# Kernel tuning notes

Measured on AMD Instinct MI355X. Metric: run time of the kernel, lower is better.

## Reference

```python
import jax, jax.numpy as jnp
import numpy as np
from jax import lax

T = 131072  # num frames
PARENTS = [-1, 0, 0, 1, 2, 3, 4, 5, 6]          # lower-body kinematic tree
LOWER_BODY = [0, 1, 2, 4, 5, 7, 8, 10, 11]      # SMPL joint ids of the 9 lower-body joints
FEET = [7, 5, 8, 6]                              # left toe, left heel, right toe, right heel (lower-body local ids)
FLOOR_Y = -0.93                                  # min y of ankle/foot joints in SMPL zero pose
GRAVITY_VELOCITY = -0.0018


def setup_inputs() -> dict:
    key = jax.random.key(0)
    k1, k2, k3 = jax.random.split(key, 3)
    pose = jax.random.normal(k1, (T, 24, 3, 3), dtype=jnp.float32)
    bone = 0.2 * jax.random.normal(k2, (9, 3), dtype=jnp.float32)
    bone = bone.at[:3].set(0.0)  # root + hip offsets zeroed, as in __init__ (b[:3] = 0)
    index = jax.random.randint(k3, (T,), 0, 4, dtype=jnp.int32)
    return {"pose": pose, "lower_body_bone": bone, "index": index}


def _forward_kinematics(pose_lower, bone):
    # pose_lower: [T, 9, 3, 3] local rotations; bone: [9, 3] bone offsets.
    # R_global[i] = R_global[parent] @ R_local[i];  p[i] = p[parent] + R_global[parent] @ bone[i]
    Rg = [pose_lower[:, 0]]
    p = [jnp.broadcast_to(bone[0], (pose_lower.shape[0], 3))]
    for i in range(1, 9):
        pa = PARENTS[i]
        Rg.append(jnp.einsum('tij,tjk->tik', Rg[pa], pose_lower[:, i]))
        p.append(p[pa] + jnp.einsum('tij,j->ti', Rg[pa], bone[i]))
    return jnp.stack(p, axis=1)  # [T, 9, 3]


def reference(pose, lower_body_bone, index):
    gravity = jnp.array([0.0, GRAVITY_VELOCITY, 0.0], dtype=pose.dtype)
    pose_lower = pose[:, jnp.array(LOWER_BODY)]               # [T, 9, 3, 3]
    j = _forward_kinematics(pose_lower, lower_body_bone)      # [T, 9, 3]

    # per-foot velocities: j[t-1] - j[t], zero at t=0  -> [T, 4, 3]
    feet = j[:, jnp.array(FEET)]                              # [T, 4, 3]
    vel_full = jnp.concatenate([jnp.zeros((1, 4, 3), dtype=j.dtype), feet[:-1] - feet[1:]], axis=0)
    vel_select = jnp.take_along_axis(vel_full, index[:, None, None].astype(jnp.int32), axis=1)[:, 0]  # [T, 3]
    velocity = gravity + vel_select                           # [T, 3]

    # sequential floor-contact correction on the y component
    foot_min_y = jnp.min(j[:, 5:9, 1], axis=1)                # [T]

    def step(root_y, inp):
        vy, fmin = inp
        foot_y = root_y + fmin
        vy_new = jnp.where(foot_y + vy <= FLOOR_Y, FLOOR_Y - foot_y, vy)
        return root_y + vy_new, vy_new

    _, vy_all = lax.scan(step, jnp.asarray(0.0, dtype=j.dtype), (velocity[:, 1], foot_min_y))
    velocity = velocity.at[:, 1].set(vy_all)

    trans = jnp.cumsum(velocity, axis=0)                      # velocity_to_root_position
    return pose, trans
```

## Files before the change

### kernel.cpp

```cpp
#include <hip/hip_runtime.h>
#include <math.h>

#define T_TOTAL   131072
#define POSE_FLTS (131072 * 216)
#define BT        64
#define NB        (T_TOTAL / BT)
#define F4PB      (BT * 54)
#define TS_LDS    84
#define FLOOR_YC  (-0.93f)
#define GRAV_Y    (-0.0018f)
#define NEG_INF   (-INFINITY)

typedef float floatx4 __attribute__((ext_vector_type(4)));


__device__ __forceinline__ void mat3mul(const float* A, const float* B, float* C) {
#pragma unroll
    for (int r = 0; r < 3; ++r) {
#pragma unroll
        for (int c = 0; c < 3; ++c) {
            C[r * 3 + c] = fmaf(A[r * 3 + 2], B[6 + c],
                           fmaf(A[r * 3 + 1], B[3 + c],
                                A[r * 3 + 0] * B[c]));
        }
    }
}

__device__ __forceinline__ void mva(const float* R, const float* b,
                                    const float* pin, float* pout) {
#pragma unroll
    for (int r = 0; r < 3; ++r) {
        pout[r] = pin[r] + fmaf(R[r * 3 + 2], b[2],
                            fmaf(R[r * 3 + 1], b[1], R[r * 3 + 0] * b[0]));
    }
}

__device__ __forceinline__ float sel_foot(const float f[12], int idx, int c) {
    float r = f[0 + c];
    r = (idx == 1) ? f[3 + c] : r;
    r = (idx == 2) ? f[6 + c] : r;
    r = (idx == 3) ? f[9 + c] : r;
    return r;
}

__device__ __forceinline__ void fk_feet(const float* __restrict__ P,
                                        const float* __restrict__ bone,
                                        float feet[12], float* fmin) {
    float Pl[84];
    const floatx4* p4 = (const floatx4*)P;
#pragma unroll
    for (int i = 0; i < 7; ++i) {
        floatx4 q = p4[i];
        Pl[4*i] = q.x; Pl[4*i+1] = q.y; Pl[4*i+2] = q.z; Pl[4*i+3] = q.w;
    }
#pragma unroll
    for (int i = 9; i < 14; ++i) {
        floatx4 q = p4[i];
        Pl[4*i] = q.x; Pl[4*i+1] = q.y; Pl[4*i+2] = q.z; Pl[4*i+3] = q.w;
    }
#pragma unroll
    for (int i = 15; i < 21; ++i) {
        floatx4 q = p4[i];
        Pl[4*i] = q.x; Pl[4*i+1] = q.y; Pl[4*i+2] = q.z; Pl[4*i+3] = q.w;
    }

    const float* M0 = Pl + 0;
    const float* M1 = Pl + 9;
    const float* M2 = Pl + 18;
    const float* M3 = Pl + 36;
    const float* M4 = Pl + 45;
    const float* M5 = Pl + 63;
    const float* M6 = Pl + 72;

    float R1[9], R2[9], R3[9], R4[9], R5[9], R6[9];
    mat3mul(M0, M1, R1);
    mat3mul(M0, M2, R2);
    mat3mul(R1, M3, R3);
    mat3mul(R2, M4, R4);
    mat3mul(R3, M5, R5);
    mat3mul(R4, M6, R6);

    float p0[3] = {bone[0], bone[1], bone[2]};
    float p1[3], p2[3], p3[3], p4a[3], p5[3], p6[3], p7[3], p8[3];
    mva(M0, bone + 3,  p0, p1);
    mva(M0, bone + 6,  p0, p2);
    mva(R1, bone + 9,  p1, p3);
    mva(R2, bone + 12, p2, p4a);
    mva(R3, bone + 15, p3, p5);
    mva(R4, bone + 18, p4a, p6);
    mva(R5, bone + 21, p5, p7);
    mva(R6, bone + 24, p6, p8);

    feet[0] = p7[0]; feet[1]  = p7[1]; feet[2]  = p7[2];
    feet[3] = p5[0]; feet[4]  = p5[1]; feet[5]  = p5[2];
    feet[6] = p8[0]; feet[7]  = p8[1]; feet[8]  = p8[2];
    feet[9] = p6[0]; feet[10] = p6[1]; feet[11] = p6[2];
    *fmin = fminf(fminf(p5[1], p6[1]), fminf(p7[1], p8[1]));
}

__device__ __forceinline__ void wave_incl_scan(float& Sx, float& Sz,
                                               float& A, float& B, int lane) {
#pragma unroll
    for (int off = 1; off < 64; off <<= 1) {
        float ox = __shfl_up(Sx, off, 64);
        float oz = __shfl_up(Sz, off, 64);
        float oA = __shfl_up(A, off, 64);
        float oB = __shfl_up(B, off, 64);
        if (lane >= off) {
            Sx += ox;
            Sz += oz;
            B = fmaxf(oB + A, B);
            A = oA + A;
        }
    }
}


__global__ __launch_bounds__(256) void k_main(const float* __restrict__ pose,
                                              const float* __restrict__ bone,
                                              const int* __restrict__ index,
                                              floatx4* __restrict__ outPose4,
                                              float4* __restrict__ vws,
                                              float4* __restrict__ wsAgg) {
    __shared__ float smem[BT * TS_LDS + 12];
    int tid = threadIdx.x, b = blockIdx.x;

    const floatx4* __restrict__ src = (const floatx4*)pose + (size_t)b * F4PB;
    floatx4*       __restrict__ dst = outPose4              + (size_t)b * F4PB;

    floatx4 r[7];
#pragma unroll
    for (int j = 0; j < 7; ++j) r[j] = src[j * 256 + tid];
#pragma unroll
    for (int j = 0; j < 7; ++j) {
        int idx = j * 256 + tid;
        __builtin_nontemporal_store(r[j], &dst[idx]);
        int tsl = idx / 54;
        int w   = idx - tsl * 54;
        if (w < 21) *(floatx4*)&smem[tsl * TS_LDS + w * 4] = r[j];
    }
#pragma unroll
    for (int j = 0; j < 6; ++j) r[j] = src[(7 + j) * 256 + tid];
#pragma unroll
    for (int j = 0; j < 6; ++j) {
        int idx = (7 + j) * 256 + tid;
        __builtin_nontemporal_store(r[j], &dst[idx]);
        int tsl = idx / 54;
        int w   = idx - tsl * 54;
        if (w < 21) *(floatx4*)&smem[tsl * TS_LDS + w * 4] = r[j];
    }
    if (tid < 128) {
        int idx = 13 * 256 + tid;
        floatx4 q = src[idx];
        __builtin_nontemporal_store(q, &dst[idx]);
        int tsl = idx / 54;
        int w   = idx - tsl * 54;
        if (w < 21) *(floatx4*)&smem[tsl * TS_LDS + w * 4] = q;
    }
    __syncthreads();

    float feet[12], fmin;
    if (tid < 64) {
        fk_feet(&smem[tid * TS_LDS], bone, feet, &fmin);
    } else if (tid == 64 && b > 0) {
        float f2[12], m2;
        fk_feet(pose + ((size_t)b * BT - 1) * 216, bone, f2, &m2);
#pragma unroll
        for (int k = 0; k < 12; ++k) smem[BT * TS_LDS + k] = f2[k];
    }
    __syncthreads();

    if (tid < 64) {
        int lane = tid;
        int t = b * BT + lane;

        float fp[12];
#pragma unroll
        for (int k = 0; k < 12; ++k) fp[k] = __shfl_up(feet[k], 1, 64);
        if (lane == 0 && b > 0) {
#pragma unroll
            for (int k = 0; k < 12; ++k) fp[k] = smem[BT * TS_LDS + k];
        }

        float vx, vy, vz;
        if (t == 0) {
            vx = 0.f; vy = GRAV_Y; vz = 0.f;
        } else {
            int idx = index[t];
            vx = sel_foot(fp, idx, 0) - sel_foot(feet, idx, 0);
            vy = GRAV_Y + sel_foot(fp, idx, 1) - sel_foot(feet, idx, 1);
            vz = sel_foot(fp, idx, 2) - sel_foot(feet, idx, 2);
        }
        float A = vy;
        float B = FLOOR_YC - fmin;
        vws[t] = make_float4(vx, vz, A, B);

        float Sx = vx, Sz = vz;
        wave_incl_scan(Sx, Sz, A, B, lane);
        if (lane == 63) wsAgg[b] = make_float4(Sx, Sz, A, B);
    }
}

__global__ __launch_bounds__(1024) void k_phase2(const float4* __restrict__ wsAgg,
                                                 float4* __restrict__ wsIn) {
    __shared__ float sx[1024], sz[1024], sa[1024], sb[1024];
    int tid = threadIdx.x;

    float4 a0 = wsAgg[2 * tid];
    float4 a1 = wsAgg[2 * tid + 1];
    float cx = a0.x + a1.x;
    float cz = a0.y + a1.y;
    float cb = fmaxf(a0.w + a1.z, a1.w);
    float ca = a0.z + a1.z;
    sx[tid] = cx; sz[tid] = cz; sa[tid] = ca; sb[tid] = cb;
    __syncthreads();

    for (int off = 1; off < 1024; off <<= 1) {
        float px = 0.f, pz = 0.f, pa = 0.f, pb = NEG_INF;
        bool h = (tid >= off);
        if (h) { px = sx[tid - off]; pz = sz[tid - off]; pa = sa[tid - off]; pb = sb[tid - off]; }
        __syncthreads();
        if (h) {
            float qa = sa[tid], qb = sb[tid];
            sx[tid] = px + sx[tid];
            sz[tid] = pz + sz[tid];
            sb[tid] = fmaxf(pb + qa, qb);
            sa[tid] = pa + qa;
        }
        __syncthreads();
    }

    float ex = 0.f, ez = 0.f, ea = 0.f, eb = NEG_INF;
    if (tid > 0) { ex = sx[tid - 1]; ez = sz[tid - 1]; ea = sa[tid - 1]; eb = sb[tid - 1]; }

    wsIn[2 * tid] = make_float4(ex, ez, fmaxf(ea, eb), 0.f);

    float fx = ex + a0.x;
    float fz = ez + a0.y;
    float fb = fmaxf(eb + a0.z, a0.w);
    float fa = ea + a0.z;
    wsIn[2 * tid + 1] = make_float4(fx, fz, fmaxf(fa, fb), 0.f);
}

__global__ __launch_bounds__(256) void k_phase3(const float4* __restrict__ vws,
                                                const float4* __restrict__ wsIn,
                                                float* __restrict__ trans) {
    int tid = threadIdx.x, bk = blockIdx.x;
    int lane = tid & 63, wv = tid >> 6;
    int u = bk * 4 + wv;
    int t = u * 64 + lane;

    float4 v = vws[t];
    float ix = v.x, iz = v.y, iA = v.z, iB = v.w;
    wave_incl_scan(ix, iz, iA, iB, lane);

    float4 bin = wsIn[u];
    trans[(size_t)t * 3 + 0] = bin.x + ix;
    trans[(size_t)t * 3 + 1] = fmaxf(bin.z + iA, iB);
    trans[(size_t)t * 3 + 2] = bin.y + iz;
}


extern "C" void kernel_launch(void* const* d_in, const int* in_sizes, int n_in,
                              void* d_out, int out_size, void* d_ws, size_t ws_size,
                              hipStream_t stream) {
    const float* pose  = (const float*)d_in[0];
    const float* bone  = (const float*)d_in[1];
    const int*   index = (const int*)d_in[2];
    float* out   = (float*)d_out;
    float* trans = out + POSE_FLTS;

    float4* vws   = (float4*)d_ws;
    float4* wsAgg = vws + T_TOTAL;
    float4* wsIn  = wsAgg + NB;

    k_main  <<<NB, 256, 0, stream>>>(pose, bone, index, (floatx4*)out, vws, wsAgg);
    k_phase2<<<1, 1024, 0, stream>>>(wsAgg, wsIn);
    k_phase3<<<T_TOTAL / 256, 256, 0, stream>>>(vws, wsIn, trans);
}
```

Before: 52.75 us.

## Transpose pose tile in LDS, load boundary frame cooperatively, store wave-scanned prefixes

The LDS staging buffer becomes a transposed, padded (feature-major, stride 65) tile. Per-thread FK reads are now conflict-free column reads instead of strided float4 rows, and the 14 loads are issued together before any stores. The previous block's last frame is loaded cooperatively by 18 threads into an extra tile column, replacing one thread's serial global gather. The main kernel now stores the wave-inclusive scan results, so phase3 no longer repeats the shuffle scan. The cost is more scalar LDS writes per float4 and more live registers.

```diff
diff --git a/kernel.cpp b/kernel.cpp
--- a/kernel.cpp
+++ b/kernel.cpp
@@ -4,9 +4,11 @@
 #define T_TOTAL   131072
 #define POSE_FLTS (131072 * 216)
 #define BT        64
-#define NB        (T_TOTAL / BT)
+#define NU        (T_TOTAL / BT)
 #define F4PB      (BT * 54)
-#define TS_LDS    84
+#define TILE_W    65
+#define TILE_F    72
+#define SCR       (TILE_F * TILE_W)
 #define FLOOR_YC  (-0.93f)
 #define GRAV_Y    (-0.0018f)
 #define NEG_INF   (-INFINITY)
@@ -43,34 +45,16 @@
     return r;
 }
 
-__device__ __forceinline__ void fk_feet(const float* __restrict__ P,
+__device__ __forceinline__ void fk_core(const float* Pl,
                                         const float* __restrict__ bone,
                                         float feet[12], float* fmin) {
-    float Pl[84];
-    const floatx4* p4 = (const floatx4*)P;
-#pragma unroll
-    for (int i = 0; i < 7; ++i) {
-        floatx4 q = p4[i];
-        Pl[4*i] = q.x; Pl[4*i+1] = q.y; Pl[4*i+2] = q.z; Pl[4*i+3] = q.w;
-    }
-#pragma unroll
-    for (int i = 9; i < 14; ++i) {
-        floatx4 q = p4[i];
-        Pl[4*i] = q.x; Pl[4*i+1] = q.y; Pl[4*i+2] = q.z; Pl[4*i+3] = q.w;
-    }
-#pragma unroll
-    for (int i = 15; i < 21; ++i) {
-        floatx4 q = p4[i];
-        Pl[4*i] = q.x; Pl[4*i+1] = q.y; Pl[4*i+2] = q.z; Pl[4*i+3] = q.w;
-    }
-
     const float* M0 = Pl + 0;
     const float* M1 = Pl + 9;
     const float* M2 = Pl + 18;
-    const float* M3 = Pl + 36;
-    const float* M4 = Pl + 45;
-    const float* M5 = Pl + 63;
-    const float* M6 = Pl + 72;
+    const float* M3 = Pl + 28;
+    const float* M4 = Pl + 37;
+    const float* M5 = Pl + 51;
+    const float* M6 = Pl + 60;
 
     float R1[9], R2[9], R3[9], R4[9], R5[9], R6[9];
     mat3mul(M0, M1, R1);
@@ -98,6 +82,15 @@
     *fmin = fminf(fminf(p5[1], p6[1]), fminf(p7[1], p8[1]));
 }
 
+__device__ __forceinline__ void fk_feet_col(const float* __restrict__ tile, int col,
+                                            const float* __restrict__ bone,
+                                            float feet[12], float* fmin) {
+    float Pl[TILE_F];
+#pragma unroll
+    for (int f = 0; f < TILE_F; ++f) Pl[f] = tile[f * TILE_W + col];
+    fk_core(Pl, bone, feet, fmin);
+}
+
 __device__ __forceinline__ void wave_incl_scan(float& Sx, float& Sz,
                                                float& A, float& B, int lane) {
 #pragma unroll
@@ -115,6 +108,21 @@
     }
 }
 
+__device__ __forceinline__ void extract_tile(float* __restrict__ tile, int idx, floatx4 q) {
+    int tsl = idx / 54;
+    int w   = idx - tsl * 54;
+    int base = -1;
+    if (w <= 6)                  base = 4 * w;
+    else if (w >= 9 && w <= 13)  base = 4 * w - 8;
+    else if (w >= 15 && w <= 20) base = 4 * w - 12;
+    if (base >= 0) {
+        tile[(base + 0) * TILE_W + tsl] = q.x;
+        tile[(base + 1) * TILE_W + tsl] = q.y;
+        tile[(base + 2) * TILE_W + tsl] = q.z;
+        tile[(base + 3) * TILE_W + tsl] = q.w;
+    }
+}
+
 
 __global__ __launch_bounds__(256) void k_main(const float* __restrict__ pose,
                                               const float* __restrict__ bone,
@@ -122,64 +130,64 @@
                                               floatx4* __restrict__ outPose4,
                                               float4* __restrict__ vws,
                                               float4* __restrict__ wsAgg) {
-    __shared__ float smem[BT * TS_LDS + 12];
-    int tid = threadIdx.x, b = blockIdx.x;
-
-    const floatx4* __restrict__ src = (const floatx4*)pose + (size_t)b * F4PB;
-    floatx4*       __restrict__ dst = outPose4              + (size_t)b * F4PB;
-
-    floatx4 r[7];
-#pragma unroll
-    for (int j = 0; j < 7; ++j) r[j] = src[j * 256 + tid];
-#pragma unroll
-    for (int j = 0; j < 7; ++j) {
+    __shared__ __align__(16) float tile[SCR + 16];
+    int tid = threadIdx.x, u = blockIdx.x;
+
+    const floatx4* __restrict__ src = (const floatx4*)pose + (size_t)u * F4PB;
+    floatx4*       __restrict__ dst = outPose4              + (size_t)u * F4PB;
+
+    floatx4 r[14];
+#pragma unroll
+    for (int j = 0; j < 13; ++j) r[j] = src[j * 256 + tid];
+    floatx4 qb;
+    bool has14   = (tid < 128);
+    bool hasBnd  = (u > 0 && tid >= 128 && tid < 128 + 18);
+    if (has14) {
+        r[13] = src[13 * 256 + tid];
+    } else if (hasBnd) {
+        int k = tid - 128;
+        int o = k + (k >= 7 ? 2 : 0) + (k >= 12 ? 1 : 0);
+        qb = *(const floatx4*)(pose + ((size_t)u * BT - 1) * 216 + o * 4);
+    }
+
+#pragma unroll
+    for (int j = 0; j < 13; ++j) {
         int idx = j * 256 + tid;
         __builtin_nontemporal_store(r[j], &dst[idx]);
-        int tsl = idx / 54;
-        int w   = idx - tsl * 54;
-        if (w < 21) *(floatx4*)&smem[tsl * TS_LDS + w * 4] = r[j];
-    }
-#pragma unroll
-    for (int j = 0; j < 6; ++j) r[j] = src[(7 + j) * 256 + tid];
-#pragma unroll
-    for (int j = 0; j < 6; ++j) {
-        int idx = (7 + j) * 256 + tid;
-        __builtin_nontemporal_store(r[j], &dst[idx]);
-        int tsl = idx / 54;
-        int w   = idx - tsl * 54;
-        if (w < 21) *(floatx4*)&smem[tsl * TS_LDS + w * 4] = r[j];
-    }
-    if (tid < 128) {
+        extract_tile(tile, idx, r[j]);
+    }
+    if (has14) {
         int idx = 13 * 256 + tid;
-        floatx4 q = src[idx];
-        __builtin_nontemporal_store(q, &dst[idx]);
-        int tsl = idx / 54;
-        int w   = idx - tsl * 54;
-        if (w < 21) *(floatx4*)&smem[tsl * TS_LDS + w * 4] = q;
+        __builtin_nontemporal_store(r[13], &dst[idx]);
+        extract_tile(tile, idx, r[13]);
+    } else if (hasBnd) {
+        int k = tid - 128;
+#pragma unroll
+        for (int i = 0; i < 4; ++i) tile[(4 * k + i) * TILE_W + 64] = qb[i];
     }
     __syncthreads();
 
-    float feet[12], fmin;
+    float feet[12], fmin = 0.f;
     if (tid < 64) {
-        fk_feet(&smem[tid * TS_LDS], bone, feet, &fmin);
-    } else if (tid == 64 && b > 0) {
+        fk_feet_col(tile, tid, bone, feet, &fmin);
+    } else if (tid == 64 && u > 0) {
         float f2[12], m2;
-        fk_feet(pose + ((size_t)b * BT - 1) * 216, bone, f2, &m2);
-#pragma unroll
-        for (int k = 0; k < 12; ++k) smem[BT * TS_LDS + k] = f2[k];
+        fk_feet_col(tile, 64, bone, f2, &m2);
+#pragma unroll
+        for (int k = 0; k < 12; ++k) tile[SCR + k] = f2[k];
     }
     __syncthreads();
 
     if (tid < 64) {
         int lane = tid;
-        int t = b * BT + lane;
+        int t = u * BT + lane;
 
         float fp[12];
 #pragma unroll
         for (int k = 0; k < 12; ++k) fp[k] = __shfl_up(feet[k], 1, 64);
-        if (lane == 0 && b > 0) {
-#pragma unroll
-            for (int k = 0; k < 12; ++k) fp[k] = smem[BT * TS_LDS + k];
+        if (lane == 0 && u > 0) {
+#pragma unroll
+            for (int k = 0; k < 12; ++k) fp[k] = tile[SCR + k];
         }
 
         float vx, vy, vz;
@@ -191,13 +199,11 @@
             vy = GRAV_Y + sel_foot(fp, idx, 1) - sel_foot(feet, idx, 1);
             vz = sel_foot(fp, idx, 2) - sel_foot(feet, idx, 2);
         }
-        float A = vy;
-        float B = FLOOR_YC - fmin;
-        vws[t] = make_float4(vx, vz, A, B);
-
-        float Sx = vx, Sz = vz;
-        wave_incl_scan(Sx, Sz, A, B, lane);
-        if (lane == 63) wsAgg[b] = make_float4(Sx, Sz, A, B);
+        float ix = vx, iz = vz, iA = vy, iB = FLOOR_YC - fmin;
+        wave_incl_scan(ix, iz, iA, iB, lane);
+
+        vws[(size_t)t] = make_float4(ix, iz, iA, iB);
+        if (lane == 63) wsAgg[u] = make_float4(ix, iz, iA, iB);
     }
 }
 
@@ -248,16 +254,13 @@
     int tid = threadIdx.x, bk = blockIdx.x;
     int lane = tid & 63, wv = tid >> 6;
     int u = bk * 4 + wv;
-    int t = u * 64 + lane;
-
-    float4 v = vws[t];
-    float ix = v.x, iz = v.y, iA = v.z, iB = v.w;
-    wave_incl_scan(ix, iz, iA, iB, lane);
-
+    size_t t = (size_t)u * 64 + lane;
+
+    float4 v   = vws[t];
     float4 bin = wsIn[u];
-    trans[(size_t)t * 3 + 0] = bin.x + ix;
-    trans[(size_t)t * 3 + 1] = fmaxf(bin.z + iA, iB);
-    trans[(size_t)t * 3 + 2] = bin.y + iz;
+    trans[t * 3 + 0] = bin.x + v.x;
+    trans[t * 3 + 1] = fmaxf(bin.z + v.z, v.w);
+    trans[t * 3 + 2] = bin.y + v.y;
 }
 
 
@@ -272,9 +275,9 @@
 
     float4* vws   = (float4*)d_ws;
     float4* wsAgg = vws + T_TOTAL;
-    float4* wsIn  = wsAgg + NB;
-
-    k_main  <<<NB, 256, 0, stream>>>(pose, bone, index, (floatx4*)out, vws, wsAgg);
+    float4* wsIn  = wsAgg + NU;
+
+    k_main  <<<NU, 256, 0, stream>>>(pose, bone, index, (floatx4*)out, vws, wsAgg);
     k_phase2<<<1, 1024, 0, stream>>>(wsAgg, wsIn);
-    k_phase3<<<T_TOTAL / 256, 256, 0, stream>>>(vws, wsIn, trans);
-}
+    k_phase3<<<NU / 4, 256, 0, stream>>>(vws, wsIn, trans);
+}
```

New measurement: 51.74 us. Within noise of the previous version (-1.9%).
